# Performance work log

Measured on AMD Instinct MI355X. Metric: run time of the kernel, lower is better.

Reference implementation:

```python
import jax, jax.numpy as jnp
import numpy as np

B, N, D, H = 4, 1024, 1024, 16
Dh = D // H


def setup_inputs() -> dict:
    key = jax.random.key(0)
    ks = jax.random.split(key, 5)
    w = 0.02
    return {
        "x": jax.random.normal(ks[0], (B, N, D), dtype=jnp.float32),
        "Wq": jax.random.normal(ks[1], (D, D), dtype=jnp.float32) * w,
        "bq": jnp.zeros((D,), dtype=jnp.float32),
        "Wk": jax.random.normal(ks[2], (D, D), dtype=jnp.float32) * w,
        "bk": jnp.zeros((D,), dtype=jnp.float32),
        "Wv": jax.random.normal(ks[3], (D, D), dtype=jnp.float32) * w,
        "bv": jnp.zeros((D,), dtype=jnp.float32),
        "Wc": jax.random.normal(ks[4], (D, D), dtype=jnp.float32) * w,
        "bc": jnp.zeros((D,), dtype=jnp.float32),
    }


def reference(x, Wq, bq, Wk, bk, Wv, bv, Wc, bc):
    # q/k/v projections: nn.Linear computes x @ W.T + b
    q = jnp.einsum("bnd,ed->bne", x, Wq) + bq
    k = jnp.einsum("bnd,ed->bne", x, Wk) + bk
    v = jnp.einsum("bnd,ed->bne", x, Wv) + bv
    # split heads: [B,N,D] -> [B,H,N,Dh]
    qh = q.reshape(B, N, H, Dh).transpose(0, 2, 1, 3)
    kh = k.reshape(B, N, H, Dh).transpose(0, 2, 1, 3)
    vh = v.reshape(B, N, H, Dh).transpose(0, 2, 1, 3)
    # NOTE (faithful quirk): original uses scale = q.size(1) = seq_len N,
    # not head_dim, so scores are scaled by N**-0.5.
    scale = jnp.float32(N) ** -0.5
    scores = jnp.einsum("bhnd,bhmd->bhnm", qh, kh) * scale  # [B,H,N,N]
    attn = jax.nn.softmax(scores, axis=-1)
    # attn_dropout = 0.0 -> identity
    o = jnp.einsum("bhnm,bhmd->bhnd", attn, vh)  # [B,H,N,Dh]
    # NOTE (faithful quirk): original does v.resize(original_size) on the
    # contiguous [B,H,N,Dh] tensor, reinterpreting memory as [B,N,D]
    # WITHOUT permuting heads back. Replicate exactly:
    o = o.reshape(B, N, D)
    out = jnp.einsum("bnd,ed->bne", o, Wc) + bc
    return out
```

## Files before the change

### kernel.cpp

```cpp
#include <hip/hip_runtime.h>
#include <cstddef>
#include <cstdint>

#define B_  4
#define N_  1024
#define D_  1024
#define H_  16
#define DH  64
#define M_  4096

typedef __attribute__((ext_vector_type(4))) float   f32x4;
typedef __attribute__((ext_vector_type(8))) __bf16  bf16x8;

#define MFMA(a, b, c) __builtin_amdgcn_mfma_f32_16x16x32_bf16((a), (b), (c), 0, 0, 0)
#define GLDS(gp, lp) __builtin_amdgcn_global_load_lds( \
    (__attribute__((address_space(1))) void*)(gp),     \
    (__attribute__((address_space(3))) void*)(lp), 16, 0, 0)

__global__ __launch_bounds__(256) void convert_k(
    const float* __restrict__ x,  const float* __restrict__ Wq,
    const float* __restrict__ Wk, const float* __restrict__ Wv,
    const float* __restrict__ Wc,
    __bf16* __restrict__ xb, __bf16* __restrict__ wqkvb,
    __bf16* __restrict__ wcb)
{
    const unsigned u = blockIdx.x * 256u + threadIdx.x;
    const unsigned e = u * 8u;
    const float* src;
    __bf16* dst;
    if (e < 4194304u) { src = x + e; dst = xb + e; }
    else {
        const unsigned t2 = e - 4194304u;
        const unsigned wsel = t2 >> 20;
        const unsigned wo = t2 & 1048575u;
        src = (wsel == 0 ? Wq : wsel == 1 ? Wk : wsel == 2 ? Wv : Wc) + wo;
        dst = (wsel < 3 ? wqkvb + (size_t)wsel * 1048576u : wcb) + wo;
    }
    const float4 f0 = *(const float4*)(src);
    const float4 f1 = *(const float4*)(src + 4);
    bf16x8 r;
    r[0] = (__bf16)f0.x; r[1] = (__bf16)f0.y; r[2] = (__bf16)f0.z; r[3] = (__bf16)f0.w;
    r[4] = (__bf16)f1.x; r[5] = (__bf16)f1.y; r[6] = (__bf16)f1.z; r[7] = (__bf16)f1.w;
    *(bf16x8*)dst = r;
}

__global__ __launch_bounds__(256, 3) void gemm_qkv(
    const __bf16* __restrict__ xb, const __bf16* __restrict__ Wb,
    const float* __restrict__ bq, const float* __restrict__ bk,
    const float* __restrict__ bv,
    __bf16* __restrict__ qk_out, __bf16* __restrict__ vT)
{
    __shared__ __bf16 As[4096];
    __shared__ __bf16 Bs[4096];

    const int tid  = threadIdx.x;
    const int w    = tid >> 6;
    const int lane = tid & 63;
    const int quad = lane >> 4;
    const int l15  = lane & 15;
    const int wr   = w >> 1, wc = w & 1;

    const int z  = blockIdx.z;
    const bool VT = (z == 2);

    int m0, n0;
    if (VT) { m0 = blockIdx.x * 128; n0 = blockIdx.y * 128; }
    else    { m0 = blockIdx.y * 128; n0 = blockIdx.x * 128; }

    const __bf16* Ap = VT ? (Wb + (size_t)2 * D_ * D_) : xb;
    const __bf16* Bp = VT ? xb : (Wb + (size_t)z * D_ * D_);

    const int c1 = w * 128 + lane, c2 = c1 + 64;
    const size_t aoff1 = (size_t)(m0 + ((c1 >> 6) * 16) + (c1 & 15)) * D_ + (((c1 >> 4) & 3) * 8);
    const size_t aoff2 = (size_t)(m0 + ((c2 >> 6) * 16) + (c2 & 15)) * D_ + (((c2 >> 4) & 3) * 8);
    const size_t boff1 = (size_t)(n0 + ((c1 >> 6) * 16) + (c1 & 15)) * D_ + (((c1 >> 4) & 3) * 8);
    const size_t boff2 = (size_t)(n0 + ((c2 >> 6) * 16) + (c2 & 15)) * D_ + (((c2 >> 4) & 3) * 8);
    __bf16* asdst1 = As + w * 1024;
    __bf16* asdst2 = As + w * 1024 + 512;
    __bf16* bsdst1 = Bs + w * 1024;
    __bf16* bsdst2 = Bs + w * 1024 + 512;

    f32x4 acc[4][4];
    #pragma unroll
    for (int i = 0; i < 4; ++i)
        #pragma unroll
        for (int j = 0; j < 4; ++j)
            acc[i][j] = (f32x4){0.f, 0.f, 0.f, 0.f};

    for (int k0 = 0; k0 < D_; k0 += 32) {
        GLDS(Ap + aoff1 + k0, asdst1);
        GLDS(Ap + aoff2 + k0, asdst2);
        GLDS(Bp + boff1 + k0, bsdst1);
        GLDS(Bp + boff2 + k0, bsdst2);
        __syncthreads();

        bf16x8 af[4], bf[4];
        #pragma unroll
        for (int t = 0; t < 4; ++t) {
            af[t] = *(const bf16x8*)(As + ((wr * 4 + t) * 64 + quad * 16 + l15) * 8);
            bf[t] = *(const bf16x8*)(Bs + ((wc * 4 + t) * 64 + quad * 16 + l15) * 8);
        }
        #pragma unroll
        for (int mt = 0; mt < 4; ++mt)
            #pragma unroll
            for (int nt = 0; nt < 4; ++nt)
                acc[mt][nt] = MFMA(af[mt], bf[nt], acc[mt][nt]);
        __syncthreads();
    }

    if (!VT) {
        const float* bias = (z == 0) ? bq : bk;
        float bvv[4];
        #pragma unroll
        for (int nt = 0; nt < 4; ++nt)
            bvv[nt] = bias[n0 + wc * 64 + nt * 16 + l15];
        __bf16* C = qk_out + (size_t)z * M_ * D_;
        #pragma unroll
        for (int mt = 0; mt < 4; ++mt) {
            #pragma unroll
            for (int r = 0; r < 4; ++r) {
                const int row = m0 + wr * 64 + mt * 16 + quad * 4 + r;
                #pragma unroll
                for (int nt = 0; nt < 4; ++nt) {
                    const int col = n0 + wc * 64 + nt * 16 + l15;
                    const size_t idx = (((size_t)(row >> 10) * H_ + (col >> 6)) * N_
                                        + (row & 1023)) * DH + (col & 63);
                    C[idx] = (__bf16)(acc[mt][nt][r] + bvv[nt]);
                }
            }
        }
    } else {
        #pragma unroll
        for (int mt = 0; mt < 4; ++mt) {
            #pragma unroll
            for (int r = 0; r < 4; ++r) {
                const int row = m0 + wr * 64 + mt * 16 + quad * 4 + r;
                const float brow = bv[row];
                #pragma unroll
                for (int nt = 0; nt < 4; ++nt) {
                    const int col = n0 + wc * 64 + nt * 16 + l15;
                    const size_t idx = (((size_t)(col >> 10) * H_ + (row >> 6)) * DH
                                        + (row & 63)) * N_ + (col & 1023);
                    vT[idx] = (__bf16)(acc[mt][nt][r] + brow);
                }
            }
        }
    }
}

__global__ __launch_bounds__(256, 6) void gemm_out(
    const __bf16* __restrict__ A0, const __bf16* __restrict__ Wb,
    const float* __restrict__ b0, float* __restrict__ Cb)
{
    __shared__ __bf16 As[2048];
    __shared__ __bf16 Bs[4096];

    const int tid  = threadIdx.x;
    const int w    = tid >> 6;
    const int lane = tid & 63;
    const int quad = lane >> 4;
    const int l15  = lane & 15;
    const int wr   = w >> 1, wc = w & 1;

    const int m0 = blockIdx.y * 64;
    const int n0 = blockIdx.x * 128;

    const int Tt = tid >> 6, ko = (tid >> 4) & 3, l = tid & 15;
    const size_t aoff  = (size_t)(m0 + Tt * 16 + l) * D_ + ko * 8;
    const size_t boff1 = (size_t)(n0 + Tt * 16 + l) * D_ + ko * 8;
    const size_t boff2 = boff1 + (size_t)64 * D_;
    __bf16* adst  = As + w * 512;
    __bf16* bdst1 = Bs + w * 512;
    __bf16* bdst2 = Bs + 2048 + w * 512;

    f32x4 acc[2][4];
    #pragma unroll
    for (int i = 0; i < 2; ++i)
        #pragma unroll
        for (int j = 0; j < 4; ++j)
            acc[i][j] = (f32x4){0.f, 0.f, 0.f, 0.f};

    for (int k0 = 0; k0 < D_; k0 += 32) {
        GLDS(A0 + aoff  + k0, adst);
        GLDS(Wb + boff1 + k0, bdst1);
        GLDS(Wb + boff2 + k0, bdst2);
        __syncthreads();

        bf16x8 af[2], bf[4];
        #pragma unroll
        for (int mt = 0; mt < 2; ++mt)
            af[mt] = *(const bf16x8*)(As + (((wr * 2 + mt) * 4 + quad) * 16 + l15) * 8);
        #pragma unroll
        for (int nt = 0; nt < 4; ++nt)
            bf[nt] = *(const bf16x8*)(Bs + (((wc * 4 + nt) * 4 + quad) * 16 + l15) * 8);
        #pragma unroll
        for (int mt = 0; mt < 2; ++mt)
            #pragma unroll
            for (int nt = 0; nt < 4; ++nt)
                acc[mt][nt] = MFMA(af[mt], bf[nt], acc[mt][nt]);
        __syncthreads();
    }

    float bvv[4];
    #pragma unroll
    for (int nt = 0; nt < 4; ++nt)
        bvv[nt] = b0[n0 + wc * 64 + nt * 16 + l15];
    #pragma unroll
    for (int mt = 0; mt < 2; ++mt) {
        #pragma unroll
        for (int r = 0; r < 4; ++r) {
            const int row = m0 + (wr * 2 + mt) * 16 + quad * 4 + r;
            #pragma unroll
            for (int nt = 0; nt < 4; ++nt) {
                const int col = n0 + wc * 64 + nt * 16 + l15;
                Cb[(size_t)row * D_ + col] = acc[mt][nt][r] + bvv[nt];
            }
        }
    }
}

#define SP  68
#define SC2 0.04508422f

__global__ __launch_bounds__(256, 4) void attn_mfma(
    const __bf16* __restrict__ qh, const __bf16* __restrict__ kh,
    const __bf16* __restrict__ vT, __bf16* __restrict__ ob)
{
    __shared__ __bf16 Ks[4096];
    __shared__ __bf16 Vs[4096];
    __shared__ float  Ps[4][16 * SP];

    const int tid  = threadIdx.x;
    const int w    = tid >> 6;
    const int lane = tid & 63;
    const int quad = lane >> 4;
    const int l15  = lane & 15;

    const int bh = blockIdx.x & 63;
    const int qt = blockIdx.x >> 6;
    const int b  = bh >> 4;
    const int h  = bh & 15;

    const __bf16* qp = qh + ((size_t)(b * H_ + h) * N_ + qt * 64 + w * 16 + l15) * DH + quad * 8;
    const bf16x8 qf0 = *(const bf16x8*)(qp);
    const bf16x8 qf1 = *(const bf16x8*)(qp + 32);

    const int c1 = tid, c2 = tid + 256;
    const int nt1 = c1 >> 7, ko1 = (c1 >> 4) & 7, l1 = c1 & 15;
    const int nt2 = c2 >> 7, ko2 = (c2 >> 4) & 7, l2 = c2 & 15;
    const __bf16* khead = kh + (size_t)(b * H_ + h) * N_ * DH;
    const __bf16* vhead = vT + (size_t)(b * H_ + h) * DH * N_;
    const size_t koff1 = (size_t)(nt1 * 16 + l1) * DH + ko1 * 8;
    const size_t koff2 = (size_t)(nt2 * 16 + l2) * DH + ko2 * 8;
    const size_t voff1 = (size_t)(nt1 * 16 + l1) * N_ + ko1 * 8;
    const size_t voff2 = (size_t)(nt2 * 16 + l2) * N_ + ko2 * 8;
    __bf16* ksdst1 = Ks + w * 512;
    __bf16* ksdst2 = Ks + 2048 + w * 512;
    __bf16* vsdst1 = Vs + w * 512;
    __bf16* vsdst2 = Vs + 2048 + w * 512;

    float psum[4] = {0.f, 0.f, 0.f, 0.f};
    f32x4 Ov[4];
    #pragma unroll
    for (int nt = 0; nt < 4; ++nt) Ov[nt] = (f32x4){0.f, 0.f, 0.f, 0.f};

    for (int kt = 0; kt < 16; ++kt) {
        GLDS(khead + (size_t)kt * 64 * DH + koff1, ksdst1);
        GLDS(khead + (size_t)kt * 64 * DH + koff2, ksdst2);
        GLDS(vhead + (size_t)kt * 64 + voff1, vsdst1);
        GLDS(vhead + (size_t)kt * 64 + voff2, vsdst2);
        __syncthreads();

        f32x4 sa[4];
        #pragma unroll
        for (int nt = 0; nt < 4; ++nt) {
            const bf16x8 kf0 = *(const bf16x8*)(Ks + (nt * 128 + quad * 16 + l15) * 8);
            const bf16x8 kf1 = *(const bf16x8*)(Ks + (nt * 128 + (quad + 4) * 16 + l15) * 8);
            sa[nt] = (f32x4){0.f, 0.f, 0.f, 0.f};
            sa[nt] = MFMA(qf0, kf0, sa[nt]);
            sa[nt] = MFMA(qf1, kf1, sa[nt]);
        }

        #pragma unroll
        for (int nt = 0; nt < 4; ++nt) {
            #pragma unroll
            for (int r = 0; r < 4; ++r) {
                const float p = __builtin_exp2f(sa[nt][r] * SC2);
                psum[r] += p;
                Ps[w][(quad * 4 + r) * SP + nt * 16 + l15] = p;
            }
        }

        #pragma unroll
        for (int kw = 0; kw < 2; ++kw) {
            const f32x4 pa = *(const f32x4*)&Ps[w][l15 * SP + kw * 32 + quad * 8];
            const f32x4 pb = *(const f32x4*)&Ps[w][l15 * SP + kw * 32 + quad * 8 + 4];
            bf16x8 pf;
            #pragma unroll
            for (int j = 0; j < 4; ++j) { pf[j] = (__bf16)pa[j]; pf[4 + j] = (__bf16)pb[j]; }
            #pragma unroll
            for (int nt = 0; nt < 4; ++nt) {
                const bf16x8 vf = *(const bf16x8*)(Vs + (nt * 128 + (kw * 4 + quad) * 16 + l15) * 8);
                Ov[nt] = MFMA(pf, vf, Ov[nt]);
            }
        }
        __syncthreads();
    }

    float lrow[4];
    #pragma unroll
    for (int r = 0; r < 4; ++r) {
        float lt = psum[r];
        lt += __shfl_xor(lt, 1);
        lt += __shfl_xor(lt, 2);
        lt += __shfl_xor(lt, 4);
        lt += __shfl_xor(lt, 8);
        lrow[r] = lt;
    }

    #pragma unroll
    for (int r = 0; r < 4; ++r) {
        const float inv = 1.0f / lrow[r];
        const int row = qt * 64 + w * 16 + quad * 4 + r;
        __bf16* op = ob + ((size_t)(b * H_ + h) * N_ + row) * DH + l15;
        #pragma unroll
        for (int nt = 0; nt < 4; ++nt)
            op[nt * 16] = (__bf16)(Ov[nt][r] * inv);
    }
}

extern "C" void kernel_launch(void* const* d_in, const int* in_sizes, int n_in,
                              void* d_out, int out_size, void* d_ws, size_t ws_size,
                              hipStream_t stream) {
    const float* x  = (const float*)d_in[0];
    const float* Wq = (const float*)d_in[1];
    const float* bq = (const float*)d_in[2];
    const float* Wk = (const float*)d_in[3];
    const float* bk = (const float*)d_in[4];
    const float* Wv = (const float*)d_in[5];
    const float* bv = (const float*)d_in[6];
    const float* Wc = (const float*)d_in[7];
    const float* bc = (const float*)d_in[8];
    float* out = (float*)d_out;

    char* base = (char*)d_ws;
    __bf16* xb    = (__bf16*)(base);
    __bf16* wqkvb = (__bf16*)(base + (size_t)8  * 1048576);
    __bf16* wcb   = (__bf16*)(base + (size_t)14 * 1048576);
    __bf16* qkvb  = (__bf16*)(base + (size_t)16 * 1048576);
    __bf16* vTb   = (__bf16*)(base + (size_t)40 * 1048576);
    __bf16* obf   = (__bf16*)(base);

    __bf16* qhb = qkvb;
    __bf16* khb = qkvb + (size_t)M_ * D_;

    convert_k<<<dim3(4096), dim3(256), 0, stream>>>(
        x, Wq, Wk, Wv, Wc, xb, wqkvb, wcb);

    gemm_qkv<<<dim3(8, 32, 3), dim3(256), 0, stream>>>(
        xb, wqkvb, bq, bk, bv, qkvb, vTb);

    attn_mfma<<<dim3(1024), dim3(256), 0, stream>>>(qhb, khb, vTb, obf);

    gemm_out<<<dim3(8, 64, 1), dim3(256), 0, stream>>>(obf, wcb, bc, out);
}
```

Baseline: 207.9 us.

## Triple-buffer LDS with async prefetch in QKV and output projection GEMMs

Replaces the single-buffer load/sync/compute loop in both projection GEMMs with a three-stage LDS ring buffer. Global-to-LDS loads for tile t+2 are issued while tile t is computed, gated by explicit vmcnt waits and one barrier per iteration instead of two. This aims to hide global memory latency behind MFMA work. It triples LDS use, so gemm_out's occupancy hint drops from 6 to 4 blocks per CU, and correctness now depends on the hand-written waitcnt counts.

Result: no change. 209.5 us (+0.8%).

```diff
diff --git a/kernel.cpp b/kernel.cpp
--- a/kernel.cpp
+++ b/kernel.cpp
@@ -50,8 +50,8 @@
     const float* __restrict__ bv,
     __bf16* __restrict__ qk_out, __bf16* __restrict__ vT)
 {
-    __shared__ __bf16 As[4096];
-    __shared__ __bf16 Bs[4096];
+    __shared__ __bf16 As[3 * 4096];
+    __shared__ __bf16 Bs[3 * 4096];
 
     const int tid  = threadIdx.x;
     const int w    = tid >> 6;
@@ -75,10 +75,8 @@
     const size_t aoff2 = (size_t)(m0 + ((c2 >> 6) * 16) + (c2 & 15)) * D_ + (((c2 >> 4) & 3) * 8);
     const size_t boff1 = (size_t)(n0 + ((c1 >> 6) * 16) + (c1 & 15)) * D_ + (((c1 >> 4) & 3) * 8);
     const size_t boff2 = (size_t)(n0 + ((c2 >> 6) * 16) + (c2 & 15)) * D_ + (((c2 >> 4) & 3) * 8);
-    __bf16* asdst1 = As + w * 1024;
-    __bf16* asdst2 = As + w * 1024 + 512;
-    __bf16* bsdst1 = Bs + w * 1024;
-    __bf16* bsdst2 = Bs + w * 1024 + 512;
+    const int so1 = w * 1024;
+    const int so2 = w * 1024 + 512;
 
     f32x4 acc[4][4];
     #pragma unroll
@@ -87,26 +85,48 @@
         for (int j = 0; j < 4; ++j)
             acc[i][j] = (f32x4){0.f, 0.f, 0.f, 0.f};
 
-    for (int k0 = 0; k0 < D_; k0 += 32) {
-        GLDS(Ap + aoff1 + k0, asdst1);
-        GLDS(Ap + aoff2 + k0, asdst2);
-        GLDS(Bp + boff1 + k0, bsdst1);
-        GLDS(Bp + boff2 + k0, bsdst2);
-        __syncthreads();
-
-        bf16x8 af[4], bf[4];
-        #pragma unroll
-        for (int t = 0; t < 4; ++t) {
-            af[t] = *(const bf16x8*)(As + ((wr * 4 + t) * 64 + quad * 16 + l15) * 8);
-            bf[t] = *(const bf16x8*)(Bs + ((wc * 4 + t) * 64 + quad * 16 + l15) * 8);
+    #define STAGE_Q(t, bi) do {                                     \
+        const size_t kq = (size_t)(t) * 32;                         \
+        __bf16* Ad = As + (bi) * 4096;                              \
+        __bf16* Bd = Bs + (bi) * 4096;                              \
+        GLDS(Ap + aoff1 + kq, Ad + so1);                            \
+        GLDS(Ap + aoff2 + kq, Ad + so2);                            \
+        GLDS(Bp + boff1 + kq, Bd + so1);                            \
+        GLDS(Bp + boff2 + kq, Bd + so2);                            \
+    } while (0)
+
+    STAGE_Q(0, 0);
+    STAGE_Q(1, 1);
+
+    int rb = 0;
+    for (int t = 0; t < 32; ++t) {
+        if (t < 31) asm volatile("s_waitcnt vmcnt(4)" ::: "memory");
+        else        asm volatile("s_waitcnt vmcnt(0)" ::: "memory");
+        __builtin_amdgcn_s_barrier();
+        asm volatile("" ::: "memory");
+
+        if (t < 30) {
+            int wb = rb + 2; if (wb >= 3) wb -= 3;
+            STAGE_Q(t + 2, wb);
+        }
+
+        const __bf16* Ar = As + rb * 4096;
+        const __bf16* Br = Bs + rb * 4096;
+        bf16x8 af[4], bfv[4];
+        #pragma unroll
+        for (int i = 0; i < 4; ++i) {
+            af[i]  = *(const bf16x8*)(Ar + ((wr * 4 + i) * 64 + quad * 16 + l15) * 8);
+            bfv[i] = *(const bf16x8*)(Br + ((wc * 4 + i) * 64 + quad * 16 + l15) * 8);
         }
         #pragma unroll
         for (int mt = 0; mt < 4; ++mt)
             #pragma unroll
             for (int nt = 0; nt < 4; ++nt)
-                acc[mt][nt] = MFMA(af[mt], bf[nt], acc[mt][nt]);
-        __syncthreads();
-    }
+                acc[mt][nt] = MFMA(af[mt], bfv[nt], acc[mt][nt]);
+
+        rb = rb + 1; if (rb == 3) rb = 0;
+    }
+    #undef STAGE_Q
 
     if (!VT) {
         const float* bias = (z == 0) ? bq : bk;
@@ -148,12 +168,12 @@
     }
 }
 
-__global__ __launch_bounds__(256, 6) void gemm_out(
+__global__ __launch_bounds__(256, 4) void gemm_out(
     const __bf16* __restrict__ A0, const __bf16* __restrict__ Wb,
     const float* __restrict__ b0, float* __restrict__ Cb)
 {
-    __shared__ __bf16 As[2048];
-    __shared__ __bf16 Bs[4096];
+    __shared__ __bf16 As[3 * 2048];
+    __shared__ __bf16 Bs[3 * 4096];
 
     const int tid  = threadIdx.x;
     const int w    = tid >> 6;
@@ -169,9 +189,6 @@
     const size_t aoff  = (size_t)(m0 + Tt * 16 + l) * D_ + ko * 8;
     const size_t boff1 = (size_t)(n0 + Tt * 16 + l) * D_ + ko * 8;
     const size_t boff2 = boff1 + (size_t)64 * D_;
-    __bf16* adst  = As + w * 512;
-    __bf16* bdst1 = Bs + w * 512;
-    __bf16* bdst2 = Bs + 2048 + w * 512;
 
     f32x4 acc[2][4];
     #pragma unroll
@@ -180,26 +197,46 @@
         for (int j = 0; j < 4; ++j)
             acc[i][j] = (f32x4){0.f, 0.f, 0.f, 0.f};
 
-    for (int k0 = 0; k0 < D_; k0 += 32) {
-        GLDS(A0 + aoff  + k0, adst);
-        GLDS(Wb + boff1 + k0, bdst1);
-        GLDS(Wb + boff2 + k0, bdst2);
-        __syncthreads();
-
-        bf16x8 af[2], bf[4];
+    #define STAGE_O(t, bi) do {                                     \
+        const size_t kq = (size_t)(t) * 32;                         \
+        GLDS(A0 + aoff  + kq, As + (bi) * 2048 + w * 512);          \
+        GLDS(Wb + boff1 + kq, Bs + (bi) * 4096 + w * 512);          \
+        GLDS(Wb + boff2 + kq, Bs + (bi) * 4096 + 2048 + w * 512);   \
+    } while (0)
+
+    STAGE_O(0, 0);
+    STAGE_O(1, 1);
+
+    int rb = 0;
+    for (int t = 0; t < 32; ++t) {
+        if (t < 31) asm volatile("s_waitcnt vmcnt(3)" ::: "memory");
+        else        asm volatile("s_waitcnt vmcnt(0)" ::: "memory");
+        __builtin_amdgcn_s_barrier();
+        asm volatile("" ::: "memory");
+
+        if (t < 30) {
+            int wb = rb + 2; if (wb >= 3) wb -= 3;
+            STAGE_O(t + 2, wb);
+        }
+
+        const __bf16* Ar = As + rb * 2048;
+        const __bf16* Br = Bs + rb * 4096;
+        bf16x8 af[2], bfv[4];
         #pragma unroll
         for (int mt = 0; mt < 2; ++mt)
-            af[mt] = *(const bf16x8*)(As + (((wr * 2 + mt) * 4 + quad) * 16 + l15) * 8);
+            af[mt] = *(const bf16x8*)(Ar + (((wr * 2 + mt) * 4 + quad) * 16 + l15) * 8);
         #pragma unroll
         for (int nt = 0; nt < 4; ++nt)
-            bf[nt] = *(const bf16x8*)(Bs + (((wc * 4 + nt) * 4 + quad) * 16 + l15) * 8);
+            bfv[nt] = *(const bf16x8*)(Br + (((wc * 4 + nt) * 4 + quad) * 16 + l15) * 8);
         #pragma unroll
         for (int mt = 0; mt < 2; ++mt)
             #pragma unroll
             for (int nt = 0; nt < 4; ++nt)
-                acc[mt][nt] = MFMA(af[mt], bf[nt], acc[mt][nt]);
-        __syncthreads();
-    }
+                acc[mt][nt] = MFMA(af[mt], bfv[nt], acc[mt][nt]);
+
+        rb = rb + 1; if (rb == 3) rb = 0;
+    }
+    #undef STAGE_O
 
     float bvv[4];
     #pragma unroll
```

## Rewrite QKV GEMM with 256x256 tiles, 8 waves and double-buffered LDS ring

Applied to the files above, without the earlier changes.

Replaces the 128x128, 4-wave QKV projection GEMM with a 256x256 tile, 512-thread kernel over a flattened grid of 192 blocks. Q and K are computed together as one 2048-wide output, and V^T gets its own block range. The K loop now uses a 64-deep, double-buffered LDS ring (128 KB) whose global-to-LDS loads are interleaved with the MFMA phases. These loads are synchronised with raw barriers, vmcnt waits and s_setprio to overlap memory traffic with compute. The aim is more operand reuse per tile and hidden load latency, at the cost of fewer blocks (192 on the device) and higher register and LDS pressure.

Result: faster. 194.0 us (-6.7%).

```diff
diff --git a/kernel.cpp b/kernel.cpp
--- a/kernel.cpp
+++ b/kernel.cpp
@@ -44,85 +44,137 @@
     *(bf16x8*)dst = r;
 }
 
-__global__ __launch_bounds__(256, 3) void gemm_qkv(
+__global__ __launch_bounds__(512, 2) void gemm_qkv256(
     const __bf16* __restrict__ xb, const __bf16* __restrict__ Wb,
     const float* __restrict__ bq, const float* __restrict__ bk,
     const float* __restrict__ bv,
     __bf16* __restrict__ qk_out, __bf16* __restrict__ vT)
 {
-    __shared__ __bf16 As[4096];
-    __shared__ __bf16 Bs[4096];
+    __shared__ __bf16 ring[65536];
 
     const int tid  = threadIdx.x;
     const int w    = tid >> 6;
     const int lane = tid & 63;
     const int quad = lane >> 4;
     const int l15  = lane & 15;
-    const int wr   = w >> 1, wc = w & 1;
-
-    const int z  = blockIdx.z;
-    const bool VT = (z == 2);
-
+    const int wr   = w >> 2;
+    const int wc   = w & 3;
+
+    const int bid = blockIdx.x;
+    const bool VT = (bid >= 128);
     int m0, n0;
-    if (VT) { m0 = blockIdx.x * 128; n0 = blockIdx.y * 128; }
-    else    { m0 = blockIdx.y * 128; n0 = blockIdx.x * 128; }
-
-    const __bf16* Ap = VT ? (Wb + (size_t)2 * D_ * D_) : xb;
-    const __bf16* Bp = VT ? xb : (Wb + (size_t)z * D_ * D_);
-
-    const int c1 = w * 128 + lane, c2 = c1 + 64;
-    const size_t aoff1 = (size_t)(m0 + ((c1 >> 6) * 16) + (c1 & 15)) * D_ + (((c1 >> 4) & 3) * 8);
-    const size_t aoff2 = (size_t)(m0 + ((c2 >> 6) * 16) + (c2 & 15)) * D_ + (((c2 >> 4) & 3) * 8);
-    const size_t boff1 = (size_t)(n0 + ((c1 >> 6) * 16) + (c1 & 15)) * D_ + (((c1 >> 4) & 3) * 8);
-    const size_t boff2 = (size_t)(n0 + ((c2 >> 6) * 16) + (c2 & 15)) * D_ + (((c2 >> 4) & 3) * 8);
-    __bf16* asdst1 = As + w * 1024;
-    __bf16* asdst2 = As + w * 1024 + 512;
-    __bf16* bsdst1 = Bs + w * 1024;
-    __bf16* bsdst2 = Bs + w * 1024 + 512;
-
-    f32x4 acc[4][4];
-    #pragma unroll
-    for (int i = 0; i < 4; ++i)
+    const __bf16 *Ap, *Bp;
+    if (!VT) { m0 = (bid >> 3) * 256; n0 = (bid & 7) * 256; Ap = xb; Bp = Wb; }
+    else {
+        const int v = bid - 128;
+        m0 = (v & 3) * 256;
+        n0 = (v >> 2) * 256;
+        Ap = Wb + (size_t)2 * D_ * D_; Bp = xb;
+    }
+
+    const size_t sgl = (size_t)(w * 16 + l15) * D_ + quad * 8;
+    const __bf16* Asrc = Ap + (size_t)m0 * D_ + sgl;
+    const __bf16* Bsrc = Bp + (size_t)n0 * D_ + sgl;
+    __bf16* const ringA = ring;
+    __bf16* const ringB = ring + 32768;
+    const int sdst = w * 1024;
+
+#define STG_A(tt, h) do {                                               \
+    const __bf16* s_ = Asrc + (size_t)(h) * 128 * D_ + (tt) * 64;       \
+    __bf16* d_ = ringA + ((((tt) & 1) * 2 + (h)) * 8192) + sdst;        \
+    GLDS(s_, d_); GLDS(s_ + 32, d_ + 512); } while (0)
+#define STG_B(tt, h) do {                                               \
+    const __bf16* s_ = Bsrc + (size_t)(h) * 128 * D_ + (tt) * 64;       \
+    __bf16* d_ = ringB + ((((tt) & 1) * 2 + (h)) * 8192) + sdst;        \
+    GLDS(s_, d_); GLDS(s_ + 32, d_ + 512); } while (0)
+
+    f32x4 acc[8][4];
+    #pragma unroll
+    for (int i = 0; i < 8; ++i)
         #pragma unroll
         for (int j = 0; j < 4; ++j)
             acc[i][j] = (f32x4){0.f, 0.f, 0.f, 0.f};
 
-    for (int k0 = 0; k0 < D_; k0 += 32) {
-        GLDS(Ap + aoff1 + k0, asdst1);
-        GLDS(Ap + aoff2 + k0, asdst2);
-        GLDS(Bp + boff1 + k0, bsdst1);
-        GLDS(Bp + boff2 + k0, bsdst2);
-        __syncthreads();
-
-        bf16x8 af[4], bf[4];
-        #pragma unroll
-        for (int t = 0; t < 4; ++t) {
-            af[t] = *(const bf16x8*)(As + ((wr * 4 + t) * 64 + quad * 16 + l15) * 8);
-            bf[t] = *(const bf16x8*)(Bs + ((wc * 4 + t) * 64 + quad * 16 + l15) * 8);
-        }
-        #pragma unroll
-        for (int mt = 0; mt < 4; ++mt)
-            #pragma unroll
-            for (int nt = 0; nt < 4; ++nt)
-                acc[mt][nt] = MFMA(af[mt], bf[nt], acc[mt][nt]);
-        __syncthreads();
-    }
+    STG_B(0, 0); STG_B(0, 1);
+    STG_A(0, 0); STG_A(0, 1);
+    STG_B(1, 0); STG_B(1, 1);
+
+    const int rdo = lane * 8;
+
+#define READ_A(q)                                                       \
+    afr[0][0] = *(const bf16x8*)(Asl + ((2*(q)  )*2 + 0)*512);          \
+    afr[0][1] = *(const bf16x8*)(Asl + ((2*(q)  )*2 + 1)*512);          \
+    afr[1][0] = *(const bf16x8*)(Asl + ((2*(q)+1)*2 + 0)*512);          \
+    afr[1][1] = *(const bf16x8*)(Asl + ((2*(q)+1)*2 + 1)*512);
+
+#define PHASE_MFMA(q)                                                   \
+    __builtin_amdgcn_s_barrier();                                       \
+    asm volatile("s_waitcnt lgkmcnt(0)" ::: "memory");                  \
+    __builtin_amdgcn_s_setprio(1);                                      \
+    _Pragma("unroll")                                                   \
+    for (int i = 0; i < 2; ++i)                                         \
+      _Pragma("unroll")                                                 \
+      for (int nt = 0; nt < 4; ++nt) {                                  \
+        acc[2*(q)+i][nt] = MFMA(afr[i][0], bfr[nt][0], acc[2*(q)+i][nt]); \
+        acc[2*(q)+i][nt] = MFMA(afr[i][1], bfr[nt][1], acc[2*(q)+i][nt]); \
+      }                                                                 \
+    __builtin_amdgcn_s_setprio(0);
+
+    for (int t = 0; t < 16; ++t) {
+        if (t < 15) asm volatile("s_waitcnt vmcnt(4)" ::: "memory");
+        else        asm volatile("s_waitcnt vmcnt(0)" ::: "memory");
+        __builtin_amdgcn_s_barrier();
+
+        const __bf16* Asl = ringA + ((t & 1) * 2 + wr) * 8192 + rdo;
+        const __bf16* Bsl = ringB + ((t & 1) * 2 + (wc >> 1)) * 8192
+                                  + (wc & 1) * 4096 + rdo;
+        bf16x8 afr[2][2], bfr[4][2];
+
+        if (t < 15) STG_A(t + 1, 0);
+        #pragma unroll
+        for (int nt = 0; nt < 4; ++nt) {
+            bfr[nt][0] = *(const bf16x8*)(Bsl + (nt * 2 + 0) * 512);
+            bfr[nt][1] = *(const bf16x8*)(Bsl + (nt * 2 + 1) * 512);
+        }
+        READ_A(0)
+        PHASE_MFMA(0)
+        __builtin_amdgcn_s_barrier();
+
+        if (t < 15) STG_A(t + 1, 1);
+        READ_A(1)
+        PHASE_MFMA(1)
+        __builtin_amdgcn_s_barrier();
+
+        if (t < 14) STG_B(t + 2, 0);
+        READ_A(2)
+        PHASE_MFMA(2)
+        __builtin_amdgcn_s_barrier();
+
+        if (t < 14) STG_B(t + 2, 1);
+        READ_A(3)
+        PHASE_MFMA(3)
+    }
+#undef STG_A
+#undef STG_B
+#undef READ_A
+#undef PHASE_MFMA
 
     if (!VT) {
-        const float* bias = (z == 0) ? bq : bk;
+        const int zq = n0 >> 10;
+        const float* bias = zq ? bk : bq;
+        const int nb = (n0 & 1023) + wc * 64;
         float bvv[4];
         #pragma unroll
-        for (int nt = 0; nt < 4; ++nt)
-            bvv[nt] = bias[n0 + wc * 64 + nt * 16 + l15];
-        __bf16* C = qk_out + (size_t)z * M_ * D_;
-        #pragma unroll
-        for (int mt = 0; mt < 4; ++mt) {
+        for (int nt = 0; nt < 4; ++nt) bvv[nt] = bias[nb + nt * 16 + l15];
+        __bf16* C = qk_out + (size_t)zq * M_ * D_;
+        #pragma unroll
+        for (int mt = 0; mt < 8; ++mt) {
             #pragma unroll
             for (int r = 0; r < 4; ++r) {
-                const int row = m0 + wr * 64 + mt * 16 + quad * 4 + r;
+                const int row = m0 + wr * 128 + mt * 16 + quad * 4 + r;
                 #pragma unroll
                 for (int nt = 0; nt < 4; ++nt) {
-                    const int col = n0 + wc * 64 + nt * 16 + l15;
+                    const int col = nb + nt * 16 + l15;
                     const size_t idx = (((size_t)(row >> 10) * H_ + (col >> 6)) * N_
                                         + (row & 1023)) * DH + (col & 63);
                     C[idx] = (__bf16)(acc[mt][nt][r] + bvv[nt]);
@@ -131,10 +183,10 @@
         }
     } else {
         #pragma unroll
-        for (int mt = 0; mt < 4; ++mt) {
+        for (int mt = 0; mt < 8; ++mt) {
             #pragma unroll
             for (int r = 0; r < 4; ++r) {
-                const int row = m0 + wr * 64 + mt * 16 + quad * 4 + r;
+                const int row = m0 + wr * 128 + mt * 16 + quad * 4 + r;
                 const float brow = bv[row];
                 #pragma unroll
                 for (int nt = 0; nt < 4; ++nt) {
@@ -357,7 +409,7 @@
     convert_k<<<dim3(4096), dim3(256), 0, stream>>>(
         x, Wq, Wk, Wv, Wc, xb, wqkvb, wcb);
 
-    gemm_qkv<<<dim3(8, 32, 3), dim3(256), 0, stream>>>(
+    gemm_qkv256<<<dim3(192), dim3(512), 0, stream>>>(
         xb, wqkvb, bq, bk, bv, qkvb, vTb);
 
     attn_mfma<<<dim3(1024), dim3(256), 0, stream>>>(qhb, khb, vTb, obf);
```
